# Kernel tuning notes

Hardware: AMD Instinct MI355X
Metric: run time of the kernel (lower is better)

## Reference

```python
import jax, jax.numpy as jnp
import numpy as np

V = 36      # nodes per graph (3 temporal x 12 spatial)
C = 3       # temporal embedding slots
S = 12      # spatial embedding slots
F0 = 1025   # input feature width
H1, H2 = 256, 64
B = 1024    # graphs
N = B * V
DEG = 8     # random in-block neighbors per node (symmetrized -> 16 avg degree)
BN_EPS = 1e-5


def _edges(k):
    # 8 random neighbors per node within its own 36-node block, symmetrized
    nbr = jax.random.randint(k, (N, DEG), 0, V)
    block = (jnp.arange(N) // V) * V
    dst = (nbr + block[:, None]).reshape(-1)
    src = jnp.repeat(jnp.arange(N), DEG)
    return jnp.stack([jnp.concatenate([src, dst]),
                      jnp.concatenate([dst, src])]).astype(jnp.int32)


def setup_inputs() -> dict:
    k = jax.random.split(jax.random.key(0), 40)
    lin = lambda kk, i, o: (jax.random.normal(kk, (i, o), jnp.float32) / np.sqrt(i)).astype(jnp.float32)
    d = {}
    d['xF'] = jax.random.normal(k[0], (N, F0), jnp.float32)
    d['xD'] = jax.random.normal(k[1], (N, F0), jnp.float32)
    d['edge_index_F'] = _edges(k[2])
    d['edge_index_D'] = _edges(k[3])
    d['TembF'] = jax.random.normal(k[4], (C, F0), jnp.float32)
    d['SembF'] = jax.random.normal(k[5], (S, F0), jnp.float32)
    d['TembD'] = jax.random.normal(k[6], (C, F0), jnp.float32)
    d['SembD'] = jax.random.normal(k[7], (S, F0), jnp.float32)
    # ChebConv K=2 weights (Theta_0, Theta_1), biases; BatchNorm gamma/beta
    d['W0F1'] = lin(k[8], F0, H1); d['W1F1'] = lin(k[9], F0, H1); d['bF1'] = jnp.zeros((H1,), jnp.float32)
    d['gF1'] = jnp.ones((H1,), jnp.float32); d['btF1'] = jnp.zeros((H1,), jnp.float32)
    d['W0F2'] = lin(k[10], H1, H2); d['W1F2'] = lin(k[11], H1, H2); d['bF2'] = jnp.zeros((H2,), jnp.float32)
    d['gF2'] = jnp.ones((H2,), jnp.float32); d['btF2'] = jnp.zeros((H2,), jnp.float32)
    d['W0D1'] = lin(k[12], F0, H1); d['W1D1'] = lin(k[13], F0, H1); d['bD1'] = jnp.zeros((H1,), jnp.float32)
    d['gD1'] = jnp.ones((H1,), jnp.float32); d['btD1'] = jnp.zeros((H1,), jnp.float32)
    d['W0D2'] = lin(k[14], H1, H2); d['W1D2'] = lin(k[15], H1, H2); d['bD2'] = jnp.zeros((H2,), jnp.float32)
    d['gD2'] = jnp.ones((H2,), jnp.float32); d['btD2'] = jnp.zeros((H2,), jnp.float32)
    # fusion linear [256->5]; branch heads are tied-at-init clones of its halves
    Wlin = lin(k[16], 2 * (2 * H2), 5)
    blin = jnp.zeros((5,), jnp.float32)
    d['WlinF'] = Wlin[:2 * H2, :]; d['blinF'] = blin
    d['WlinD'] = Wlin[2 * H2:, :]; d['blinD'] = blin
    d['Wlin'] = Wlin; d['blin'] = blin
    return d


def _cheb(x, ei, W0, W1, b):
    # PyG ChebConv K=2, sym norm, lambda_max=2: out = x@W0 + (L_hat x)@W1 + b,
    # L_hat = -D^{-1/2} A D^{-1/2}. Transform-then-aggregate (linear, cheaper).
    n = x.shape[0]
    src, dst = ei[0], ei[1]
    deg = jax.ops.segment_sum(jnp.ones(src.shape, jnp.float32), src, n)
    dinv = jnp.where(deg > 0, jax.lax.rsqrt(jnp.maximum(deg, 1.0)), 0.0)
    w = -(dinv[src] * dinv[dst])                       # [E]
    h1 = x @ W1                                        # [N, out]
    tx1 = jax.ops.segment_sum(w[:, None] * h1[src], dst, n)  # scatter-add
    return x @ W0 + tx1 + b


def _bn_relu(x, g, bt):
    mu = x.mean(0)
    var = x.var(0)  # biased, as torch BatchNorm1d training-mode normalization
    return jax.nn.relu((x - mu) * jax.lax.rsqrt(var + BN_EPS) * g + bt)


def _branch(x, ei, Temb, Semb, W0a, W1a, ba, ga, bta, W0b, W1b, bb, gb, btb):
    n = x.shape[0]
    bsz = n // V
    x = x.reshape(bsz, C, S, F0).transpose(0, 2, 1, 3)      # [B,12,3,1025]
    x = x + Temb[None, None, :, :] + Semb[None, :, None, :]
    x = x.transpose(0, 2, 1, 3).reshape(n, F0)
    x = _bn_relu(_cheb(x, ei, W0a, W1a, ba), ga, bta)
    x = _bn_relu(_cheb(x, ei, W0b, W1b, bb), gb, btb)        # [N,64]
    # rows 12..23 of each 36-node block, pooled per graph
    idx = (jnp.arange(bsz)[:, None] * V + S + jnp.arange(S)[None, :]).reshape(-1)
    seg = jnp.repeat(jnp.arange(bsz), S)
    xs = x[idx]
    mx = jax.ops.segment_max(xs, seg, bsz)
    mn = jax.ops.segment_sum(xs, seg, bsz) / float(S)
    return jnp.concatenate([mx, mn], axis=1)                 # [B,128]


def reference(xF, xD, edge_index_F, edge_index_D, TembF, SembF, TembD, SembD,
              W0F1, W1F1, bF1, gF1, btF1, W0F2, W1F2, bF2, gF2, btF2,
              W0D1, W1D1, bD1, gD1, btD1, W0D2, W1D2, bD2, gD2, btD2,
              WlinF, blinF, WlinD, blinD, Wlin, blin):
    featF = _branch(xF, edge_index_F, TembF, SembF, W0F1, W1F1, bF1, gF1, btF1,
                    W0F2, W1F2, bF2, gF2, btF2)
    featD = _branch(xD, edge_index_D, TembD, SembD, W0D1, W1D1, bD1, gD1, btD1,
                    W0D2, W1D2, bD2, gD2, btD2)
    outF = jax.nn.softmax(featF @ WlinF + blinF, axis=-1)
    outD = jax.nn.softmax(featD @ WlinD + blinD, axis=-1)
    fusion = jnp.concatenate([featF, featD], axis=1)
    out = jax.nn.softmax(fusion @ Wlin + blin, axis=-1)
    return (outF, outD, fusion, out)
```

## Files before the change

kernel.cpp:

```cpp
#include <hip/hip_runtime.h>
#include <math.h>

#define NN    36864
#define F0    1025
#define H1D   256
#define H2D   64
#define VV    36
#define SS    12
#define BSZ   1024
#define BN_EPS 1e-5f

#define KT1   17
#define EMB_LD 1088
#define WT1_STRIDE  ((size_t)4*17*8192)
#define WT2_STRIDE  ((size_t)4*8192)

typedef __bf16 bf16x8 __attribute__((ext_vector_type(8)));
typedef __bf16 bf16x4 __attribute__((ext_vector_type(4)));
typedef float  f32x4  __attribute__((ext_vector_type(4)));

__device__ __forceinline__ float4 ld4u(const float* p) {
    float4 v;
    __builtin_memcpy(&v, p, 16);
    return v;
}

__global__ void k_zero(float* __restrict__ p, int n) {
    int i = blockIdx.x * blockDim.x + threadIdx.x;
    if (i < n) p[i] = 0.f;
}

__global__ void k_deginit(float* __restrict__ degAll) {
    int br = blockIdx.y;
    int i = blockIdx.x * 256 + threadIdx.x;
    if (i < NN) degAll[(size_t)br * NN + i] = 8.f;
}

__global__ void k_deg(const int* __restrict__ eiF, const int* __restrict__ eiD,
                      int Eh, float* __restrict__ degAll) {
    int br = blockIdx.y;
    const int* src = (br ? eiD : eiF) + Eh;
    float* deg = degAll + (size_t)br * NN;
    int e = blockIdx.x * blockDim.x + threadIdx.x;
    if (e < Eh) atomicAdd(&deg[src[e]], 1.f);
}

__device__ __forceinline__ float dinv_f(float d) {
    return d > 0.f ? rsqrtf(fmaxf(d, 1.f)) : 0.f;
}

__global__ void k_scatter(const int* __restrict__ eiF, const int* __restrict__ eiD,
                          int E, const float* __restrict__ degAll, float* __restrict__ AdjAll) {
    int br = blockIdx.y;
    const int* src = br ? eiD : eiF;
    const int* dst = src + E;
    const float* deg = degAll + (size_t)br * NN;
    float* Adj = AdjAll + (size_t)br * BSZ * (VV * VV);
    int e = blockIdx.x * blockDim.x + threadIdx.x;
    if (e >= E) return;
    int s = src[e], d = dst[e];
    float w = -dinv_f(deg[s]) * dinv_f(deg[d]);
    int blk = s / VV;
    atomicAdd(&Adj[(size_t)blk * (VV * VV) + (d - blk * VV) * VV + (s - blk * VV)], w);
}

__global__ __launch_bounds__(256) void k_prepEmb(
    const float* __restrict__ TembF, const float* __restrict__ SembF,
    const float* __restrict__ TembD, const float* __restrict__ SembD,
    float* __restrict__ embSAll) {
    int br = blockIdx.y;
    const float* Temb = br ? TembD : TembF;
    const float* Semb = br ? SembD : SembF;
    float* out = embSAll + (size_t)br * VV * EMB_LD;
    int id = blockIdx.x * 256 + threadIdx.x;
    if (id >= VV * (EMB_LD / 4)) return;
    int lv = id / (EMB_LD / 4);
    int k0 = (id - lv * (EMB_LD / 4)) * 4;
    const float* pt = Temb + (size_t)(lv / SS) * F0;
    const float* ps = Semb + (size_t)(lv % SS) * F0;
    float4 v;
    float* vp = (float*)&v;
#pragma unroll
    for (int j = 0; j < 4; ++j) {
        int k = k0 + j;
        vp[j] = (k < F0) ? (pt[k] + ps[k]) : 0.f;
    }
    *reinterpret_cast<float4*>(out + (size_t)lv * EMB_LD + k0) = v;
}

__global__ __launch_bounds__(256) void k_prepW(
    const float* __restrict__ WaF, const float* __restrict__ WbF,
    const float* __restrict__ WaD, const float* __restrict__ WbD,
    __bf16* __restrict__ Wt, int K, int nkt, int split, int ldw, size_t brStride) {
    int br = blockIdx.y;
    const float* Wa = br ? WaD : WaF;
    const float* Wb = br ? WbD : WbF;
    __bf16* out = Wt + (size_t)br * brStride;

    int id = blockIdx.x * 256 + threadIdx.x;
    int gpc = nkt * 8;
    int c = id / gpc, gi = id - c * gpc;
    int kt = gi >> 3, g = gi & 7;
    int k0 = kt * 64 + g * 8;
    const float* src = (c < split) ? (Wa + c) : (Wb + (c - split));
    bf16x8 ov;
#pragma unroll
    for (int j = 0; j < 8; ++j) {
        int k = k0 + j;
        float v = (k < K) ? src[(size_t)k * ldw] : 0.f;
        ov[j] = (__bf16)v;
    }
    int r = c & 127, bn = c >> 7;
    size_t dst = ((size_t)(bn * nkt + kt) << 13) + r * 64 + ((g ^ (r & 7)) << 3);
    *(bf16x8*)(out + dst) = ov;
}

__global__ __launch_bounds__(512) void k_gemm1f(
    const float* __restrict__ xF, const float* __restrict__ xD,
    const float* __restrict__ embSAll,
    const __bf16* __restrict__ Wt1All,
    __bf16* __restrict__ H0All, __bf16* __restrict__ H1All) {
    __shared__ __align__(16) __bf16 As[2 * 8192];
    __shared__ __align__(16) __bf16 Bs[2 * 16384];
    const int tid = threadIdx.x;
    const int lane = tid & 63, wid = tid >> 6;

    const int flat = blockIdx.x;
    const int w = (flat & 7) * 144 + (flat >> 3);
    const int cy = w & 1;
    const int t2 = w >> 1;
    const int bm = t2 % 288;
    const int br = t2 / 288;

    const float* x    = br ? xD : xF;
    const float* embS = embSAll + (size_t)br * VV * EMB_LD;
    const __bf16* Wt = Wt1All + (size_t)br * WT1_STRIDE;
    __bf16* H0 = H0All + (size_t)br * NN * H1D;
    __bf16* H1 = H1All + (size_t)br * NN * H1D;

    const int wr = wid >> 2, wc = wid & 3;
    const int l15 = lane & 15, lg = lane >> 4;
    const int bn0 = cy * 2;

    const int kc = (lane & 15) * 4;
    const float *px[4], *pe[4];
    int dso[4];
#pragma unroll
    for (int i = 0; i < 4; ++i) {
        int r = wid * 16 + i * 4 + (lane >> 4);
        int g = bm * 128 + r;
        int lv = g % VV;
        px[i] = x + (size_t)g * F0 + kc;
        pe[i] = embS + (size_t)lv * EMB_LD + kc;
        dso[i] = r * 64 + (((kc >> 3) ^ (r & 7)) << 3) + (kc & 4);
    }

    int offA[2][4], offB[2][4];
#pragma unroll
    for (int kk = 0; kk < 2; ++kk) {
#pragma unroll
        for (int m = 0; m < 4; ++m) {
            int rowA = wr * 64 + m * 16 + l15;
            offA[kk][m] = rowA * 64 + (((kk * 4 + lg) ^ (rowA & 7)) << 3);
        }
#pragma unroll
        for (int n = 0; n < 4; ++n) {
            int col = wc * 64 + n * 16 + l15;
            offB[kk][n] = (col >> 7) * 8192 + (col & 127) * 64
                          + (((kk * 4 + lg) ^ (col & 7)) << 3);
        }
    }

    f32x4 acc[4][4];
#pragma unroll
    for (int m = 0; m < 4; ++m)
#pragma unroll
        for (int n = 0; n < 4; ++n) acc[m][n] = (f32x4){0.f, 0.f, 0.f, 0.f};

    f32x4 xa[4];

    auto issueX = [&](int kt) {
        int ko = kt * 64, kb = ko + kc;
#pragma unroll
        for (int i = 0; i < 4; ++i) {
            if (kb + 3 < F0) {
                float4 a = ld4u(px[i] + ko);
                xa[i] = (f32x4){a.x, a.y, a.z, a.w};
            } else {
                f32x4 v = {0.f, 0.f, 0.f, 0.f};
#pragma unroll
                for (int j = 0; j < 4; ++j)
                    if (kb + j < F0) v[j] = px[i][ko + j];
                xa[i] = v;
            }
        }
    };
    auto writeA = [&](int kt, int buf) {
        int ko = kt * 64;
#pragma unroll
        for (int i = 0; i < 4; ++i) {
            float4 e = *reinterpret_cast<const float4*>(pe[i] + ko);
            bf16x4 wv;
            wv[0] = (__bf16)(xa[i][0] + e.x);
            wv[1] = (__bf16)(xa[i][1] + e.y);
            wv[2] = (__bf16)(xa[i][2] + e.z);
            wv[3] = (__bf16)(xa[i][3] + e.w);
            *(bf16x4*)(As + buf * 8192 + dso[i]) = wv;
        }
    };
    auto issueB = [&](int kt, int buf) {
#pragma unroll
        for (int cc = 0; cc < 4; ++cc) {
            int q = (wid * 4 + cc) * 512;
            int h = q >> 13, qi = q & 8191;
            const __bf16* src = Wt + (((size_t)(bn0 + h) * KT1 + kt) << 13)
                                + qi + (lane << 3);
            __builtin_amdgcn_global_load_lds(
                (const __attribute__((address_space(1))) void*)src,
                (__attribute__((address_space(3))) void*)(Bs + buf * 16384 + q), 16, 0, 0);
        }
    };

    issueB(0, 0);
    issueX(0);
    writeA(0, 0);

    for (int kt = 0; kt < KT1; ++kt) {
        const int cur = kt & 1, nxt = cur ^ 1;
        __syncthreads();
        if (kt + 1 < KT1) {
            issueB(kt + 1, nxt);
            issueX(kt + 1);
        }
        const __bf16* Ab = As + cur * 8192;
        const __bf16* Bb = Bs + cur * 16384;
#pragma unroll
        for (int kk = 0; kk < 2; ++kk) {
            bf16x8 af[4], bb[4];
#pragma unroll
            for (int m = 0; m < 4; ++m) af[m] = *(const bf16x8*)(Ab + offA[kk][m]);
#pragma unroll
            for (int n = 0; n < 4; ++n) bb[n] = *(const bf16x8*)(Bb + offB[kk][n]);
#pragma unroll
            for (int m = 0; m < 4; ++m)
#pragma unroll
                for (int n = 0; n < 4; ++n)
                    acc[m][n] = __builtin_amdgcn_mfma_f32_16x16x32_bf16(
                        af[m], bb[n], acc[m][n], 0, 0, 0);
        }
        if (kt + 1 < KT1) writeA(kt + 1, nxt);
    }

    const int cr = lg * 4;
#pragma unroll
    for (int m = 0; m < 4; ++m) {
        int grow = bm * 128 + wr * 64 + m * 16 + cr;
#pragma unroll
        for (int n = 0; n < 4; ++n) {
            int gc = cy * 256 + wc * 64 + n * 16 + l15;
#pragma unroll
            for (int j = 0; j < 4; ++j) {
                int r = grow + j;
                if (gc < 256) H0[(size_t)r * H1D + gc] = (__bf16)acc[m][n][j];
                else          H1[(size_t)r * H1D + (gc - 256)] = (__bf16)acc[m][n][j];
            }
        }
    }
}

__global__ __launch_bounds__(256, 2) void k_gemm2f(
    const __bf16* __restrict__ YAll, const float* __restrict__ coefAll,
    const __bf16* __restrict__ Wt2All,
    float* __restrict__ G0All, __bf16* __restrict__ G1All) {
    __shared__ __align__(16) __bf16 As[2 * 8192];
    __shared__ __align__(16) __bf16 Bs[2 * 8192];
    const int tid = threadIdx.x;
    const int lane = tid & 63, wid = tid >> 6;
    const int bm = blockIdx.x, br = blockIdx.z;
    const __bf16* Y   = YAll + (size_t)br * NN * H1D;
    const float* coef = coefAll + (size_t)br * 2 * H1D;
    const __bf16* Wt  = Wt2All + (size_t)br * WT2_STRIDE;
    float*  G0 = G0All + (size_t)br * NN * H2D;
    __bf16* G1 = G1All + (size_t)br * NN * H2D;

    const int wr = wid >> 1, wc = wid & 1;
    const int l15 = lane & 15, lg = lane >> 4;

    const int kc = (lane & 15) * 4;
    const __bf16* pyr[8];
    int dso[8];
#pragma unroll
    for (int i = 0; i < 8; ++i) {
        int r = wid * 32 + i * 4 + (lane >> 4);
        pyr[i] = Y + (size_t)(bm * 128 + r) * H1D + kc;
        dso[i] = r * 64 + (((kc >> 3) ^ (r & 7)) << 3) + (kc & 4);
    }

    int offA[2][4], offB[2][4];
#pragma unroll
    for (int kk = 0; kk < 2; ++kk)
#pragma unroll
        for (int m = 0; m < 4; ++m) {
            int rowA = wr * 64 + m * 16 + l15;
            offA[kk][m] = rowA * 64 + (((kk * 4 + lg) ^ (rowA & 7)) << 3);
            int col = wc * 64 + m * 16 + l15;
            offB[kk][m] = col * 64 + (((kk * 4 + lg) ^ (col & 7)) << 3);
        }

    f32x4 acc[4][4];
#pragma unroll
    for (int m = 0; m < 4; ++m)
#pragma unroll
        for (int n = 0; n < 4; ++n) acc[m][n] = (f32x4){0.f, 0.f, 0.f, 0.f};

    bf16x4 ya[8];

    auto issueY = [&](int kt) {
        int k0 = kt * 64;
#pragma unroll
        for (int i = 0; i < 8; ++i)
            ya[i] = *reinterpret_cast<const bf16x4*>(pyr[i] + k0);
    };
    auto writeA = [&](int kt, int buf) {
        int k0 = kt * 64;
        float4 cA = *reinterpret_cast<const float4*>(coef + k0 + kc);
        float4 cB = *reinterpret_cast<const float4*>(coef + H1D + k0 + kc);
#pragma unroll
        for (int i = 0; i < 8; ++i) {
            bf16x4 wv;
            wv[0] = (__bf16)fmaxf(fmaf((float)ya[i][0], cA.x, cB.x), 0.f);
            wv[1] = (__bf16)fmaxf(fmaf((float)ya[i][1], cA.y, cB.y), 0.f);
            wv[2] = (__bf16)fmaxf(fmaf((float)ya[i][2], cA.z, cB.z), 0.f);
            wv[3] = (__bf16)fmaxf(fmaf((float)ya[i][3], cA.w, cB.w), 0.f);
            *(bf16x4*)(As + buf * 8192 + dso[i]) = wv;
        }
    };
    auto issueB = [&](int kt, int buf) {
#pragma unroll
        for (int cc = 0; cc < 4; ++cc) {
            int q = (wid * 4 + cc) * 512;
            const __bf16* src = Wt + ((size_t)kt << 13) + q + (lane << 3);
            __builtin_amdgcn_global_load_lds(
                (const __attribute__((address_space(1))) void*)src,
                (__attribute__((address_space(3))) void*)(Bs + buf * 8192 + q), 16, 0, 0);
        }
    };

    issueB(0, 0);
    issueY(0);
    writeA(0, 0);

    for (int kt = 0; kt < 4; ++kt) {
        const int cur = kt & 1, nxt = cur ^ 1;
        __syncthreads();
        if (kt + 1 < 4) {
            issueB(kt + 1, nxt);
            issueY(kt + 1);
        }
        const __bf16* Ab = As + cur * 8192;
        const __bf16* Bb = Bs + cur * 8192;
#pragma unroll
        for (int kk = 0; kk < 2; ++kk) {
            bf16x8 af[4], bb[4];
#pragma unroll
            for (int m = 0; m < 4; ++m) af[m] = *(const bf16x8*)(Ab + offA[kk][m]);
#pragma unroll
            for (int n = 0; n < 4; ++n) bb[n] = *(const bf16x8*)(Bb + offB[kk][n]);
#pragma unroll
            for (int m = 0; m < 4; ++m)
#pragma unroll
                for (int n = 0; n < 4; ++n)
                    acc[m][n] = __builtin_amdgcn_mfma_f32_16x16x32_bf16(
                        af[m], bb[n], acc[m][n], 0, 0, 0);
        }
        if (kt + 1 < 4) writeA(kt + 1, nxt);
    }

    const int cr = lg * 4;
#pragma unroll
    for (int m = 0; m < 4; ++m) {
        int grow = bm * 128 + wr * 64 + m * 16 + cr;
#pragma unroll
        for (int n = 0; n < 4; ++n) {
            int col = wc * 64 + n * 16 + l15;
#pragma unroll
            for (int j = 0; j < 4; ++j) {
                int r = grow + j;
                if (col < 64) G0[(size_t)r * H2D + col] = acc[m][n][j];
                else          G1[(size_t)r * H2D + (col - 64)] = (__bf16)acc[m][n][j];
            }
        }
    }
}

__global__ __launch_bounds__(256) void k_combine_stats1(
    const float* __restrict__ AdjAll, const __bf16* __restrict__ H1All,
    const float* __restrict__ bF, const float* __restrict__ bD,
    __bf16* __restrict__ YAll, float* __restrict__ stAll) {
    __shared__ float Adj_s[VV * VV];
    __shared__ float red[256 * 9];
    int b = blockIdx.x, br = blockIdx.y, t = threadIdx.x;
    const float* Adj = AdjAll + ((size_t)br * BSZ + b) * (VV * VV);
    const __bf16* h1 = H1All + ((size_t)br * NN + (size_t)b * VV) * H1D;
    __bf16* yb = YAll + ((size_t)br * NN + (size_t)b * VV) * H1D;
    float* st = stAll + (size_t)br * 2 * H1D;
    const float* bias = br ? bD : bF;

    for (int e = t; e < VV * VV; e += 256) Adj_s[e] = Adj[e];
    __syncthreads();

    int c0 = (t & 63) * 4, r0 = t >> 6;
    float4 bv = *reinterpret_cast<const float4*>(bias + c0);
    float acc[9][4];
#pragma unroll
    for (int i = 0; i < 9; ++i) {
        bf16x4 y = *reinterpret_cast<const bf16x4*>(yb + (size_t)(r0 + 4 * i) * H1D + c0);
        acc[i][0] = (float)y[0] + bv.x; acc[i][1] = (float)y[1] + bv.y;
        acc[i][2] = (float)y[2] + bv.z; acc[i][3] = (float)y[3] + bv.w;
    }
#pragma unroll 4
    for (int j = 0; j < VV; ++j) {
        bf16x4 hv = *reinterpret_cast<const bf16x4*>(h1 + (size_t)j * H1D + c0);
        float h0 = (float)hv[0], h1f = (float)hv[1], h2 = (float)hv[2], h3 = (float)hv[3];
#pragma unroll
        for (int i = 0; i < 9; ++i) {
            float a = Adj_s[(r0 + 4 * i) * VV + j];
            acc[i][0] = fmaf(a, h0, acc[i][0]);
            acc[i][1] = fmaf(a, h1f, acc[i][1]);
            acc[i][2] = fmaf(a, h2, acc[i][2]);
            acc[i][3] = fmaf(a, h3, acc[i][3]);
        }
    }
    float s[4] = {0, 0, 0, 0}, s2[4] = {0, 0, 0, 0};
#pragma unroll
    for (int i = 0; i < 9; ++i) {
        bf16x4 wv;
        wv[0] = (__bf16)acc[i][0]; wv[1] = (__bf16)acc[i][1];
        wv[2] = (__bf16)acc[i][2]; wv[3] = (__bf16)acc[i][3];
        *reinterpret_cast<bf16x4*>(yb + (size_t)(r0 + 4 * i) * H1D + c0) = wv;
#pragma unroll
        for (int k = 0; k < 4; ++k) { s[k] += acc[i][k]; s2[k] += acc[i][k] * acc[i][k]; }
    }
#pragma unroll
    for (int k = 0; k < 4; ++k) { red[t * 9 + k] = s[k]; red[t * 9 + 4 + k] = s2[k]; }
    __syncthreads();
    {
        int cg = t >> 2, k = t & 3;
        float ss = 0.f, ss2 = 0.f;
#pragma unroll
        for (int q = 0; q < 4; ++q) {
            ss  += red[(q * 64 + cg) * 9 + k];
            ss2 += red[(q * 64 + cg) * 9 + 4 + k];
        }
        atomicAdd(&st[t], ss);
        atomicAdd(&st[H1D + t], ss2);
    }
}

__global__ __launch_bounds__(256) void k_combine_stats2(
    const float* __restrict__ AdjAll, const __bf16* __restrict__ G1All,
    const float* __restrict__ bF, const float* __restrict__ bD,
    float* __restrict__ YAll, float* __restrict__ stAll) {
    __shared__ float Adj_s[VV * VV];
    __shared__ float red[256 * 9];
    int b = blockIdx.x, br = blockIdx.y, t = threadIdx.x;
    const float* Adj = AdjAll + ((size_t)br * BSZ + b) * (VV * VV);
    const __bf16* g1 = G1All + ((size_t)br * NN + (size_t)b * VV) * H2D;
    float* yb = YAll + ((size_t)br * NN + (size_t)b * VV) * H2D;
    float* st = stAll + (size_t)br * 2 * H2D;
    const float* bias = br ? bD : bF;

    for (int e = t; e < VV * VV; e += 256) Adj_s[e] = Adj[e];
    __syncthreads();

    int c0 = (t & 15) * 4, r0 = t >> 4;
    int nr = (r0 < 4) ? 3 : 2;
    float4 bv = *reinterpret_cast<const float4*>(bias + c0);
    float acc[3][4];
    for (int i = 0; i < nr; ++i) {
        float4 y = *reinterpret_cast<const float4*>(yb + (size_t)(r0 + 16 * i) * H2D + c0);
        acc[i][0] = y.x + bv.x; acc[i][1] = y.y + bv.y;
        acc[i][2] = y.z + bv.z; acc[i][3] = y.w + bv.w;
    }
#pragma unroll 4
    for (int j = 0; j < VV; ++j) {
        bf16x4 hv = *reinterpret_cast<const bf16x4*>(g1 + (size_t)j * H2D + c0);
        float h0 = (float)hv[0], h1f = (float)hv[1], h2 = (float)hv[2], h3 = (float)hv[3];
        for (int i = 0; i < nr; ++i) {
            float a = Adj_s[(r0 + 16 * i) * VV + j];
            acc[i][0] = fmaf(a, h0, acc[i][0]);
            acc[i][1] = fmaf(a, h1f, acc[i][1]);
            acc[i][2] = fmaf(a, h2, acc[i][2]);
            acc[i][3] = fmaf(a, h3, acc[i][3]);
        }
    }
    float s[4] = {0, 0, 0, 0}, s2[4] = {0, 0, 0, 0};
    for (int i = 0; i < nr; ++i) {
        *reinterpret_cast<float4*>(yb + (size_t)(r0 + 16 * i) * H2D + c0) =
            make_float4(acc[i][0], acc[i][1], acc[i][2], acc[i][3]);
#pragma unroll
        for (int k = 0; k < 4; ++k) { s[k] += acc[i][k]; s2[k] += acc[i][k] * acc[i][k]; }
    }
#pragma unroll
    for (int k = 0; k < 4; ++k) { red[t * 9 + k] = s[k]; red[t * 9 + 4 + k] = s2[k]; }
    __syncthreads();
    if (t < 2 * H2D) {
        int cg = (t & 63) >> 2, k = t & 3, which = t >> 6;
        float ss = 0.f;
#pragma unroll
        for (int q = 0; q < 16; ++q) ss += red[(q * 16 + cg) * 9 + which * 4 + k];
        atomicAdd(&st[(t >> 6) * H2D + (t & 63)], ss);
    }
}

__global__ void k_fin(const float* __restrict__ stAll,
                      const float* __restrict__ gF, const float* __restrict__ btF,
                      const float* __restrict__ gD, const float* __restrict__ btD,
                      float* __restrict__ coefAll, int H) {
    int br = blockIdx.x, t = threadIdx.x;
    const float* st = stAll + (size_t)br * 2 * H;
    float* coef = coefAll + (size_t)br * 2 * H;
    const float* g = br ? gD : gF;
    const float* bt = br ? btD : btF;
    if (t >= H) return;
    float mu = st[t] / (float)NN;
    float var = st[H + t] / (float)NN - mu * mu;
    float sA = g[t] * rsqrtf(var + BN_EPS);
    coef[t] = sA;
    coef[H + t] = bt[t] - mu * sA;
}

__global__ __launch_bounds__(64) void k_pool(const float* __restrict__ Y2All,
                                             const float* __restrict__ coefAll,
                                             float* __restrict__ featF,
                                             float* __restrict__ featD) {
    int b = blockIdx.x, br = blockIdx.y, c = threadIdx.x;
    const float* Y2 = Y2All + (size_t)br * NN * H2D;
    const float* coef = coefAll + (size_t)br * 2 * H2D;
    float* feat = br ? featD : featF;
    float sA = coef[c], sB = coef[H2D + c];
    float mx = -1e30f, sm = 0.f;
    const float* yb = Y2 + ((size_t)b * VV + SS) * H2D + c;
#pragma unroll
    for (int i = 0; i < SS; ++i) {
        float v = fmaxf(fmaf(yb[i * H2D], sA, sB), 0.f);
        mx = fmaxf(mx, v);
        sm += v;
    }
    feat[b * 128 + c] = mx;
    feat[b * 128 + 64 + c] = sm * (1.f / 12.f);
}

__global__ __launch_bounds__(128) void k_heads(
    const float* __restrict__ featF, const float* __restrict__ featD,
    const float* __restrict__ WlinF, const float* __restrict__ blinF,
    const float* __restrict__ WlinD, const float* __restrict__ blinD,
    const float* __restrict__ Wlin, const float* __restrict__ blin,
    float* __restrict__ out) {
    __shared__ float sF[128], sD[128], lg[24];
    int r = blockIdx.x, t = threadIdx.x;
    sF[t] = featF[r * 128 + t];
    sD[t] = featD[r * 128 + t];
    __syncthreads();
    float* fus = out + 10240 + (size_t)r * 256;
    fus[t] = sF[t];
    fus[128 + t] = sD[t];
    if (t < 5) {
        float a = blinF[t];
        for (int k = 0; k < 128; ++k) a += sF[k] * WlinF[k * 5 + t];
        lg[t] = a;
    } else if (t >= 8 && t < 13) {
        int j = t - 8;
        float a = blinD[j];
        for (int k = 0; k < 128; ++k) a += sD[k] * WlinD[k * 5 + j];
        lg[8 + j] = a;
    } else if (t >= 16 && t < 21) {
        int j = t - 16;
        float a = blin[j];
        for (int k = 0; k < 128; ++k) a += sF[k] * Wlin[k * 5 + j];
        for (int k = 0; k < 128; ++k) a += sD[k] * Wlin[(128 + k) * 5 + j];
        lg[16 + j] = a;
    }
    __syncthreads();
    if (t < 15) {
        int grp = t / 5, j = t % 5;
        const float* l = &lg[grp * 8];
        float m = l[0];
#pragma unroll
        for (int k = 1; k < 5; ++k) m = fmaxf(m, l[k]);
        float den = 0.f;
#pragma unroll
        for (int k = 0; k < 5; ++k) den += expf(l[k] - m);
        float v = expf(l[j] - m) / den;
        float* dst = (grp == 0) ? out : (grp == 1 ? out + 5120 : out + 272384);
        dst[r * 5 + j] = v;
    }
}

extern "C" void kernel_launch(void* const* d_in, const int* in_sizes, int n_in,
                              void* d_out, int out_size, void* d_ws, size_t ws_size,
                              hipStream_t stream) {
    const float* xF    = (const float*)d_in[0];
    const float* xD    = (const float*)d_in[1];
    const int*   eiF   = (const int*)d_in[2];
    const int*   eiD   = (const int*)d_in[3];
    const float* TembF = (const float*)d_in[4];
    const float* SembF = (const float*)d_in[5];
    const float* TembD = (const float*)d_in[6];
    const float* SembD = (const float*)d_in[7];
    const float* W0F1  = (const float*)d_in[8];
    const float* W1F1  = (const float*)d_in[9];
    const float* bF1   = (const float*)d_in[10];
    const float* gF1   = (const float*)d_in[11];
    const float* btF1  = (const float*)d_in[12];
    const float* W0F2  = (const float*)d_in[13];
    const float* W1F2  = (const float*)d_in[14];
    const float* bF2   = (const float*)d_in[15];
    const float* gF2   = (const float*)d_in[16];
    const float* btF2  = (const float*)d_in[17];
    const float* W0D1  = (const float*)d_in[18];
    const float* W1D1  = (const float*)d_in[19];
    const float* bD1   = (const float*)d_in[20];
    const float* gD1   = (const float*)d_in[21];
    const float* btD1  = (const float*)d_in[22];
    const float* W0D2  = (const float*)d_in[23];
    const float* W1D2  = (const float*)d_in[24];
    const float* bD2   = (const float*)d_in[25];
    const float* gD2   = (const float*)d_in[26];
    const float* btD2  = (const float*)d_in[27];
    const float* WlinF = (const float*)d_in[28];
    const float* blinF = (const float*)d_in[29];
    const float* WlinD = (const float*)d_in[30];
    const float* blinD = (const float*)d_in[31];
    const float* Wlin  = (const float*)d_in[32];
    const float* blin  = (const float*)d_in[33];

    const int E = in_sizes[2] / 2;

    float* ws = (float*)d_ws;
    size_t o = 0;
    __bf16* H0bf = (__bf16*)(ws + o);   o += (size_t)2 * NN * H1D / 2;
    __bf16* H1bf = (__bf16*)(ws + o);   o += (size_t)2 * NN * H1D / 2;
    float*  G0   = ws + o;              o += (size_t)2 * NN * H2D;
    __bf16* G1bf = (__bf16*)(ws + o);   o += (size_t)2 * NN * H2D / 2;
    __bf16* Wt1  = (__bf16*)(ws + o);   o += (size_t)2 * WT1_STRIDE / 2;
    __bf16* Wt2  = (__bf16*)(ws + o);   o += (size_t)2 * WT2_STRIDE / 2;
    float*  embS = ws + o;              o += (size_t)2 * VV * EMB_LD;
    float*  Adj  = ws + o;              o += (size_t)2 * BSZ * VV * VV;
    float*  st1  = ws + o;              o += 2 * 2 * H1D;
    float*  st2  = ws + o;              o += 2 * 2 * H2D;
    float*  deg  = ws + o;              o += (size_t)2 * NN;
    float*  coef1 = ws + o;             o += 2 * 2 * H1D;
    float*  coef2 = ws + o;             o += 2 * 2 * H2D;
    float*  featF = ws + o;             o += (size_t)BSZ * 128;
    float*  featD = ws + o;             o += (size_t)BSZ * 128;

    const int zeroN = 2 * (BSZ * VV * VV + 2 * H1D + 2 * H2D);

    k_zero<<<(zeroN + 255) / 256, 256, 0, stream>>>(Adj, zeroN);
    k_deginit<<<dim3(144, 2), 256, 0, stream>>>(deg);
    k_deg<<<dim3((E / 2 + 255) / 256, 2), 256, 0, stream>>>(eiF, eiD, E / 2, deg);
    k_scatter<<<dim3((E + 255) / 256, 2), 256, 0, stream>>>(eiF, eiD, E, deg, Adj);
    k_prepEmb<<<dim3(39, 2), 256, 0, stream>>>(TembF, SembF, TembD, SembD, embS);
    k_prepW<<<dim3(272, 2), 256, 0, stream>>>(W0F1, W1F1, W0D1, W1D1, Wt1,
                                              F0, 17, 256, H1D, WT1_STRIDE);
    k_prepW<<<dim3(16, 2), 256, 0, stream>>>(W0F2, W1F2, W0D2, W1D2, Wt2,
                                             H1D, 4, 64, H2D, WT2_STRIDE);
    k_gemm1f<<<dim3(1152), 512, 0, stream>>>(xF, xD, embS, Wt1, H0bf, H1bf);
    k_combine_stats1<<<dim3(BSZ, 2), 256, 0, stream>>>(Adj, H1bf, bF1, bD1, H0bf, st1);
    k_fin<<<dim3(2), 256, 0, stream>>>(st1, gF1, btF1, gD1, btD1, coef1, H1D);
    k_gemm2f<<<dim3(288, 1, 2), 256, 0, stream>>>(H0bf, coef1, Wt2, G0, G1bf);
    k_combine_stats2<<<dim3(BSZ, 2), 256, 0, stream>>>(Adj, G1bf, bF2, bD2, G0, st2);
    k_fin<<<dim3(2), 64, 0, stream>>>(st2, gF2, btF2, gD2, btD2, coef2, H2D);
    k_pool<<<dim3(BSZ, 2), 64, 0, stream>>>(G0, coef2, featF, featD);
    k_heads<<<BSZ, 128, 0, stream>>>(featF, featD, WlinF, blinF, WlinD, blinD,
                                     Wlin, blin, (float*)d_out);
}
```

Baseline: 461.3 us.

## Prefetch activations two tiles ahead with register double-buffering in both GEMMs

Both GEMM kernels now hold activation tiles in two register sets, loading tile k+2 while tile k+1 is written to shared memory and tile k is multiplied. The embedding load also moves into the issue phase, so its latency is hidden along with the x load. The loop is unrolled by two with fixed buffer indices. The intent is to hide global load latency that was exposed when writeA waited on loads issued in the same iteration. The cost is more live registers, which could lower occupancy.

```diff
diff --git a/kernel.cpp b/kernel.cpp
--- a/kernel.cpp
+++ b/kernel.cpp
@@ -177,12 +177,14 @@
 #pragma unroll
         for (int n = 0; n < 4; ++n) acc[m][n] = (f32x4){0.f, 0.f, 0.f, 0.f};
 
-    f32x4 xa[4];
-
-    auto issueX = [&](int kt) {
+    f32x4 xa0[4], xa1[4];
+    float4 ea0[4], ea1[4];
+
+    auto issueX = [&](int kt, f32x4 (&xa)[4], float4 (&ea)[4]) {
         int ko = kt * 64, kb = ko + kc;
 #pragma unroll
         for (int i = 0; i < 4; ++i) {
+            ea[i] = *reinterpret_cast<const float4*>(pe[i] + ko);
             if (kb + 3 < F0) {
                 float4 a = ld4u(px[i] + ko);
                 xa[i] = (f32x4){a.x, a.y, a.z, a.w};
@@ -195,16 +197,14 @@
             }
         }
     };
-    auto writeA = [&](int kt, int buf) {
-        int ko = kt * 64;
+    auto writeA = [&](int buf, f32x4 (&xa)[4], float4 (&ea)[4]) {
 #pragma unroll
         for (int i = 0; i < 4; ++i) {
-            float4 e = *reinterpret_cast<const float4*>(pe[i] + ko);
             bf16x4 wv;
-            wv[0] = (__bf16)(xa[i][0] + e.x);
-            wv[1] = (__bf16)(xa[i][1] + e.y);
-            wv[2] = (__bf16)(xa[i][2] + e.z);
-            wv[3] = (__bf16)(xa[i][3] + e.w);
+            wv[0] = (__bf16)(xa[i][0] + ea[i].x);
+            wv[1] = (__bf16)(xa[i][1] + ea[i].y);
+            wv[2] = (__bf16)(xa[i][2] + ea[i].z);
+            wv[3] = (__bf16)(xa[i][3] + ea[i].w);
             *(bf16x4*)(As + buf * 8192 + dso[i]) = wv;
         }
     };
@@ -220,18 +220,7 @@
                 (__attribute__((address_space(3))) void*)(Bs + buf * 16384 + q), 16, 0, 0);
         }
     };
-
-    issueB(0, 0);
-    issueX(0);
-    writeA(0, 0);
-
-    for (int kt = 0; kt < KT1; ++kt) {
-        const int cur = kt & 1, nxt = cur ^ 1;
-        __syncthreads();
-        if (kt + 1 < KT1) {
-            issueB(kt + 1, nxt);
-            issueX(kt + 1);
-        }
+    auto mfmaStep = [&](int cur) {
         const __bf16* Ab = As + cur * 8192;
         const __bf16* Bb = Bs + cur * 16384;
 #pragma unroll
@@ -248,7 +237,25 @@
                     acc[m][n] = __builtin_amdgcn_mfma_f32_16x16x32_bf16(
                         af[m], bb[n], acc[m][n], 0, 0, 0);
         }
-        if (kt + 1 < KT1) writeA(kt + 1, nxt);
+    };
+
+    issueX(0, xa0, ea0);
+    issueB(0, 0);
+    writeA(0, xa0, ea0);
+    issueX(1, xa1, ea1);
+
+    for (int kt = 0; kt < KT1; kt += 2) {
+        __syncthreads();
+        if (kt + 1 < KT1) issueB(kt + 1, 1);
+        if (kt + 2 < KT1) issueX(kt + 2, xa0, ea0);
+        if (kt + 1 < KT1) writeA(1, xa1, ea1);
+        mfmaStep(0);
+        if (kt + 1 >= KT1) break;
+        __syncthreads();
+        if (kt + 2 < KT1) issueB(kt + 2, 0);
+        if (kt + 3 < KT1) issueX(kt + 3, xa1, ea1);
+        if (kt + 2 < KT1) writeA(0, xa0, ea0);
+        mfmaStep(1);
     }
 
     const int cr = lg * 4;
@@ -313,15 +320,15 @@
 #pragma unroll
         for (int n = 0; n < 4; ++n) acc[m][n] = (f32x4){0.f, 0.f, 0.f, 0.f};
 
-    bf16x4 ya[8];
-
-    auto issueY = [&](int kt) {
+    bf16x4 ya0[8], ya1[8];
+
+    auto issueY = [&](int kt, bf16x4 (&ya)[8]) {
         int k0 = kt * 64;
 #pragma unroll
         for (int i = 0; i < 8; ++i)
             ya[i] = *reinterpret_cast<const bf16x4*>(pyr[i] + k0);
     };
-    auto writeA = [&](int kt, int buf) {
+    auto writeA = [&](int kt, int buf, bf16x4 (&ya)[8]) {
         int k0 = kt * 64;
         float4 cA = *reinterpret_cast<const float4*>(coef + k0 + kc);
         float4 cB = *reinterpret_cast<const float4*>(coef + H1D + k0 + kc);
@@ -345,18 +352,7 @@
                 (__attribute__((address_space(3))) void*)(Bs + buf * 8192 + q), 16, 0, 0);
         }
     };
-
-    issueB(0, 0);
-    issueY(0);
-    writeA(0, 0);
-
-    for (int kt = 0; kt < 4; ++kt) {
-        const int cur = kt & 1, nxt = cur ^ 1;
-        __syncthreads();
-        if (kt + 1 < 4) {
-            issueB(kt + 1, nxt);
-            issueY(kt + 1);
-        }
+    auto mfmaStep = [&](int cur) {
         const __bf16* Ab = As + cur * 8192;
         const __bf16* Bb = Bs + cur * 8192;
 #pragma unroll
@@ -373,7 +369,25 @@
                     acc[m][n] = __builtin_amdgcn_mfma_f32_16x16x32_bf16(
                         af[m], bb[n], acc[m][n], 0, 0, 0);
         }
-        if (kt + 1 < 4) writeA(kt + 1, nxt);
+    };
+
+    issueY(0, ya0);
+    issueB(0, 0);
+    writeA(0, 0, ya0);
+    issueY(1, ya1);
+
+    for (int kt = 0; kt < 4; kt += 2) {
+        __syncthreads();
+        if (kt + 1 < 4) issueB(kt + 1, 1);
+        if (kt + 2 < 4) issueY(kt + 2, ya0);
+        if (kt + 1 < 4) writeA(kt + 1, 1, ya1);
+        mfmaStep(0);
+        if (kt + 1 >= 4) break;
+        __syncthreads();
+        if (kt + 2 < 4) issueB(kt + 2, 0);
+        if (kt + 3 < 4) issueY(kt + 3, ya1);
+        if (kt + 2 < 4) writeA(kt + 2, 0, ya0);
+        mfmaStep(1);
     }
 
     const int cr = lg * 4;
```

Result: slower. 682.5 us (+48.0%).
